# Kernel tuning notes

Hardware: AMD Instinct MI355X
Metric: run time of the kernel (lower is better)

## Reference

```python
import jax, jax.numpy as jnp
import numpy as np

N = 50000
E = 800000
IN_DIM = 128
HID = 128
HEADS = 8
OUT_DIM = 64
NEG_SLOPE = 0.2


def setup_inputs() -> dict:
    key = jax.random.key(0)
    ks = jax.random.split(key, 10)
    x = jax.random.normal(ks[0], (N, IN_DIM), dtype=jnp.float32)
    edge_index = jax.random.randint(ks[1], (2, E), 0, N, dtype=jnp.int64)
    c1 = HID // HEADS  # 16 per-head channels, layer 1
    # layer 1 params (GATConv: lin has no bias; att_src/att_dst are [1,H,C])
    W1 = jax.random.normal(ks[2], (IN_DIM, HEADS * c1), dtype=jnp.float32) * 0.1
    att_src1 = jax.random.normal(ks[3], (1, HEADS, c1), dtype=jnp.float32) * 0.1
    att_dst1 = jax.random.normal(ks[4], (1, HEADS, c1), dtype=jnp.float32) * 0.1
    b1 = jnp.zeros((HEADS * c1,), dtype=jnp.float32)  # concat=True -> bias size H*C
    # layer 2 params (heads=1, concat=False)
    W2 = jax.random.normal(ks[5], (HID, OUT_DIM), dtype=jnp.float32) * 0.1
    att_src2 = jax.random.normal(ks[6], (1, 1, OUT_DIM), dtype=jnp.float32) * 0.1
    att_dst2 = jax.random.normal(ks[7], (1, 1, OUT_DIM), dtype=jnp.float32) * 0.1
    b2 = jnp.zeros((OUT_DIM,), dtype=jnp.float32)
    return {"x": x, "edge_index": edge_index,
            "W1": W1, "att_src1": att_src1, "att_dst1": att_dst1, "b1": b1,
            "W2": W2, "att_src2": att_src2, "att_dst2": att_dst2, "b2": b2}


def _gat_conv(x, src, dst, W, att_src, att_dst, bias, heads, concat):
    n = x.shape[0]
    c = W.shape[1] // heads
    h = (x @ W).reshape(n, heads, c)                      # [N,H,C]
    a_src = jnp.sum(h * att_src, axis=-1)                 # [N,H]
    a_dst = jnp.sum(h * att_dst, axis=-1)                 # [N,H]
    e = a_src[src] + a_dst[dst]                           # [E,H]
    e = jnp.where(e > 0, e, NEG_SLOPE * e)                # leaky_relu
    # segment softmax over incoming edges of each dst node
    m = jax.ops.segment_max(e, dst, num_segments=n)       # [N,H]
    ex = jnp.exp(e - m[dst])
    denom = jax.ops.segment_sum(ex, dst, num_segments=n)  # [N,H]
    alpha = ex / (denom[dst] + 1e-16)                     # [E,H]
    msg = h[src] * alpha[:, :, None]                      # [E,H,C]
    out = jax.ops.segment_sum(msg, dst, num_segments=n)   # [N,H,C]
    out = out.reshape(n, heads * c) if concat else out.mean(axis=1)
    return out + bias


def reference(x, edge_index, W1, att_src1, att_dst1, b1, W2, att_src2, att_dst2, b2):
    # add self-loops (PyG GATConv default add_self_loops=True)
    loops = jnp.arange(N, dtype=edge_index.dtype)
    src = jnp.concatenate([edge_index[0], loops])
    dst = jnp.concatenate([edge_index[1], loops])
    h = _gat_conv(x, src, dst, W1, att_src1, att_dst1, b1, HEADS, True)
    h = jax.nn.elu(h)
    out = _gat_conv(h, src, dst, W2, att_src2, att_dst2, b2, 1, False)
    return jax.nn.log_softmax(out, axis=1)
```

## Files before the change

### kernel.cpp

```cpp
#include <hip/hip_runtime.h>
#include <math.h>

#define N_NODES 50000
#define E_EDGES 800000
#define ET      (E_EDGES + N_NODES)
#define IN_DIM  128
#define HID     128
#define HEADS   8
#define C1      16
#define OUT_DIM 64
#define NEG_SLOPE 0.2f
#define LOG2E   1.4426950408889634f

#define TILE    8192
#define NT      ((ET + TILE - 1) / TILE)
#define NB      ((N_NODES + 255) / 256)

#define CONV_BLOCKS (N_NODES * IN_DIM / 4 / 256)
#define PREP_BLOCKS 112
#define MEGA_A (NT + CONV_BLOCKS + PREP_BLOCKS)
#define L1T_BLOCKS ((N_NODES + 63) / 64)
#define MEGA_B (NB + L1T_BLOCKS)

typedef unsigned int uint32;
typedef __attribute__((ext_vector_type(8))) short bf16x8;
typedef __attribute__((ext_vector_type(4))) float f32x4;

static __device__ __forceinline__ unsigned short f2bf(float f) {
    uint32 u = __float_as_uint(f);
    u += 0x7FFFu + ((u >> 16) & 1u);
    return (unsigned short)(u >> 16);
}


__global__ __launch_bounds__(256) void prep_all(
        const int* __restrict__ dst, int* __restrict__ cnt,
        const float* __restrict__ x, unsigned short* __restrict__ xb,
        const float* __restrict__ W1, const float* __restrict__ as1,
        const float* __restrict__ ad1, const float* __restrict__ W2,
        const float* __restrict__ as2, const float* __restrict__ ad2,
        unsigned short* __restrict__ w1t, unsigned short* __restrict__ p1t,
        unsigned short* __restrict__ w2t, unsigned short* __restrict__ p2t) {
    __shared__ int hist[NB];
    int blk = blockIdx.x, t = threadIdx.x;
    if (blk < NT) {
        for (int b = t; b < NB; b += 256) hist[b] = 0;
        __syncthreads();
        int base = blk * TILE;
        #pragma unroll
        for (int it = 0; it < TILE / 256; ++it) {
            int i = base + it * 256 + t;
            if (i < ET) {
                int d = (i < E_EDGES) ? dst[i] : (i - E_EDGES);
                atomicAdd(&hist[d >> 8], 1);
            }
        }
        __syncthreads();
        for (int b = t; b < NB; b += 256) cnt[blk * NB + b] = hist[b];
    } else if (blk < NT + CONV_BLOCKS) {
        int i = (blk - NT) * 256 + t;
        float4 v = ((const float4*)x)[i];
        ushort4 o;
        o.x = f2bf(v.x); o.y = f2bf(v.y); o.z = f2bf(v.z); o.w = f2bf(v.w);
        ((ushort4*)xb)[i] = o;
    } else {
        int b = blk - NT - CONV_BLOCKS;
        if (b < 64) {
            int i = b * 256 + t;
            int n = i >> 7, k = i & 127;
            w1t[n * IN_DIM + k] = f2bf(W1[k * HID + n]);
        } else if (b < 96) {
            int i = (b - 64) * 256 + t;
            int n = i >> 7, k = i & 127;
            w2t[n * HID + k] = f2bf(W2[k * OUT_DIM + n]);
        } else if (b < 104) {
            int i = (b - 96) * 256 + t;
            int j = i >> 7, k = i & 127;
            int hh = j & 7;
            const float* a = (j < 8) ? as1 : ad1;
            float acc = 0.f;
            #pragma unroll
            for (int c = 0; c < C1; ++c)
                acc = fmaf(W1[k * HID + hh * C1 + c], a[hh * C1 + c], acc);
            p1t[j * IN_DIM + k] = f2bf(acc * LOG2E);
        } else {
            int i = (b - 104) * 256 + t;
            int j = i >> 7, k = i & 127;
            if (j < 2) {
                const float* a = (j == 0) ? as2 : ad2;
                float acc = 0.f;
                #pragma unroll
                for (int c = 0; c < OUT_DIM; ++c)
                    acc = fmaf(W2[k * OUT_DIM + c], a[c], acc);
                p2t[j * HID + k] = f2bf(acc * LOG2E);
            } else {
                p2t[j * HID + k] = 0;
            }
        }
    }
}

__global__ __launch_bounds__(256) void bucket_scan(
        const int* __restrict__ cnt, int* __restrict__ tileOff ,
        int* __restrict__ bucketStart ) {
    __shared__ int s[256];
    int t = threadIdx.x;
    int total = 0;
    if (t < NB) {
        int run = 0;
        for (int k = 0; k < NT; ++k) {
            int c = cnt[k * NB + t];
            tileOff[k * NB + t] = run;
            run += c;
        }
        total = run;
    }
    s[t] = total;
    __syncthreads();
    #pragma unroll
    for (int off = 1; off < 256; off <<= 1) {
        int add = (t >= off) ? s[t - off] : 0;
        __syncthreads();
        s[t] += add;
        __syncthreads();
    }
    if (t < NB) bucketStart[t] = s[t] - total;
    if (t == 0) bucketStart[NB] = ET;
}

__global__ __launch_bounds__(256) void bucket_scatter(
        const int* __restrict__ src, const int* __restrict__ dst,
        const int* __restrict__ tileOff, const int* __restrict__ bucketStart,
        int2* __restrict__ pairs) {
    __shared__ int cur[NB];
    int t = threadIdx.x;
    for (int b = t; b < NB; b += 256)
        cur[b] = bucketStart[b] + tileOff[blockIdx.x * NB + b];
    __syncthreads();
    int base = blockIdx.x * TILE;
    #pragma unroll
    for (int it = 0; it < TILE / 256; ++it) {
        int i = base + it * 256 + t;
        if (i < ET) {
            int s, d;
            if (i < E_EDGES) { s = src[i]; d = dst[i]; }
            else             { s = d = i - E_EDGES; }
            int pos = atomicAdd(&cur[d >> 8], 1);
            pairs[pos] = make_int2(s, d);
        }
    }
}


__global__ __launch_bounds__(256) void build_l1t(
        const int2* __restrict__ pairs, const int* __restrict__ bucketStart,
        int* __restrict__ row_start, int* __restrict__ csr_src,
        const unsigned short* __restrict__ xb, const unsigned short* __restrict__ w1t,
        const unsigned short* __restrict__ p1t, unsigned short* __restrict__ h1b,
        float* __restrict__ a_src, float* __restrict__ a_dst) {
    __shared__ int sdeg[256];
    __shared__ int sscan[256];
    int t = threadIdx.x;
    if (blockIdx.x < NB) {
        int b = blockIdx.x;
        int beg = bucketStart[b], end = bucketStart[b + 1];
        sdeg[t] = 0;
        __syncthreads();
        for (int j = beg + t; j < end; j += 256)
            atomicAdd(&sdeg[pairs[j].y & 255], 1);
        __syncthreads();
        int v = sdeg[t];
        sscan[t] = v;
        __syncthreads();
        #pragma unroll
        for (int off = 1; off < 256; off <<= 1) {
            int add = (t >= off) ? sscan[t - off] : 0;
            __syncthreads();
            sscan[t] += add;
            __syncthreads();
        }
        int pos0 = beg + sscan[t] - v;
        int n = b * 256 + t;
        if (n < N_NODES) row_start[n] = pos0;
        if (b == 0 && t == 0) row_start[N_NODES] = ET;
        __syncthreads();
        sscan[t] = pos0;
        __syncthreads();
        for (int j = beg + t; j < end; j += 256) {
            int2 p = pairs[j];
            int pos = atomicAdd(&sscan[p.y & 255], 1);
            csr_src[pos] = p.x;
        }
        return;
    }
    int bb = blockIdx.x - NB;
    int w = t >> 6, lane = t & 63;
    int l15 = lane & 15, quad = lane >> 4;
    int n0 = bb * 64 + w * 16;
    int mrow = n0 + l15;
    int mload = (mrow < N_NODES) ? mrow : (N_NODES - 1);

    bf16x8 af[4];
    #pragma unroll
    for (int s = 0; s < 4; ++s)
        af[s] = *(const bf16x8*)&xb[(size_t)mload * IN_DIM + s * 32 + quad * 8];

    #pragma unroll
    for (int tt = 0; tt < 9; ++tt) {
        const unsigned short* Brow = (tt < 8) ? &w1t[(tt * 16 + l15) * IN_DIM]
                                              : &p1t[l15 * IN_DIM];
        f32x4 acc = {0.f, 0.f, 0.f, 0.f};
        #pragma unroll
        for (int s = 0; s < 4; ++s) {
            bf16x8 bf = *(const bf16x8*)&Brow[s * 32 + quad * 8];
            acc = __builtin_amdgcn_mfma_f32_16x16x32_bf16(af[s], bf, acc, 0, 0, 0);
        }
        int nodeb = n0 + quad * 4;
        if (tt < 8) {
            int ch = tt * 16 + l15;
            #pragma unroll
            for (int r = 0; r < 4; ++r)
                if (nodeb + r < N_NODES)
                    h1b[(size_t)(nodeb + r) * HID + ch] = f2bf(acc[r]);
        } else {
            #pragma unroll
            for (int r = 0; r < 4; ++r) {
                if (nodeb + r < N_NODES) {
                    if (l15 < 8) a_src[(nodeb + r) * HEADS + l15] = acc[r];
                    else         a_dst[(nodeb + r) * HEADS + (l15 - 8)] = acc[r];
                }
            }
        }
    }
}


__global__ __launch_bounds__(128) void l1_aggregate(
        const unsigned short* __restrict__ h1b, const float* __restrict__ a_src,
        const float* __restrict__ a_dst, const int* __restrict__ row_start,
        const int* __restrict__ csr_src, const float* __restrict__ b1,
        unsigned short* __restrict__ h_act_b) {
    int w = threadIdx.x >> 6;
    int lane = threadIdx.x & 63;
    int n = blockIdx.x * 2 + w;
    int c0 = lane * 2;
    int h = lane >> 3;
    int beg = row_start[n], end = row_start[n + 1];
    float adst = a_dst[n * HEADS + h];
    float l = 0.f, accx = 0.f, accy = 0.f;

    auto update = [&](float e, uint32 u) {
        float vx = __uint_as_float(u << 16);
        float vy = __uint_as_float(u & 0xFFFF0000u);
        e += adst;
        e = fmaxf(e, NEG_SLOPE * e);
        float p = exp2f(e);
        l += p;
        accx = fmaf(p, vx, accx);
        accy = fmaf(p, vy, accy);
    };

    int j = beg;
    for (; j + 8 <= end; j += 8) {
        int ss[8];
        #pragma unroll
        for (int q = 0; q < 8; ++q) ss[q] = csr_src[j + q];
        float ee[8]; uint32 uu[8];
        #pragma unroll
        for (int q = 0; q < 8; ++q) ee[q] = a_src[ss[q] * HEADS + h];
        #pragma unroll
        for (int q = 0; q < 8; ++q) uu[q] = *(const uint32*)&h1b[(size_t)ss[q] * HID + c0];
        #pragma unroll
        for (int q = 0; q < 8; ++q) update(ee[q], uu[q]);
    }
    for (; j + 4 <= end; j += 4) {
        int ss[4];
        #pragma unroll
        for (int q = 0; q < 4; ++q) ss[q] = csr_src[j + q];
        float ee[4]; uint32 uu[4];
        #pragma unroll
        for (int q = 0; q < 4; ++q) ee[q] = a_src[ss[q] * HEADS + h];
        #pragma unroll
        for (int q = 0; q < 4; ++q) uu[q] = *(const uint32*)&h1b[(size_t)ss[q] * HID + c0];
        #pragma unroll
        for (int q = 0; q < 4; ++q) update(ee[q], uu[q]);
    }
    for (; j < end; ++j) {
        int s = csr_src[j];
        float e = a_src[s * HEADS + h];
        uint32 u = *(const uint32*)&h1b[(size_t)s * HID + c0];
        update(e, u);
    }

    float inv = 1.f / (l + 1e-16f);
    float vx = accx * inv + b1[c0];
    float vy = accy * inv + b1[c0 + 1];
    vx = vx > 0.f ? vx : (__expf(vx) - 1.f);
    vy = vy > 0.f ? vy : (__expf(vy) - 1.f);
    uint32 packed = (uint32)f2bf(vx) | ((uint32)f2bf(vy) << 16);
    *(uint32*)&h_act_b[(size_t)n * HID + c0] = packed;
}


__global__ __launch_bounds__(256) void l2_transform_mfma(
        const unsigned short* __restrict__ h_act_b, const unsigned short* __restrict__ w2t,
        const unsigned short* __restrict__ p2t, unsigned short* __restrict__ h2b,
        float* __restrict__ a_src2, float* __restrict__ a_dst2) {
    int t = threadIdx.x, w = t >> 6, lane = t & 63;
    int l15 = lane & 15, quad = lane >> 4;
    int n0 = blockIdx.x * 64 + w * 16;
    int mrow = n0 + l15;
    int mload = (mrow < N_NODES) ? mrow : (N_NODES - 1);

    bf16x8 af[4];
    #pragma unroll
    for (int s = 0; s < 4; ++s)
        af[s] = *(const bf16x8*)&h_act_b[(size_t)mload * HID + s * 32 + quad * 8];

    #pragma unroll
    for (int tt = 0; tt < 5; ++tt) {
        const unsigned short* Brow = (tt < 4) ? &w2t[(tt * 16 + l15) * HID]
                                              : &p2t[l15 * HID];
        f32x4 acc = {0.f, 0.f, 0.f, 0.f};
        #pragma unroll
        for (int s = 0; s < 4; ++s) {
            bf16x8 bf = *(const bf16x8*)&Brow[s * 32 + quad * 8];
            acc = __builtin_amdgcn_mfma_f32_16x16x32_bf16(af[s], bf, acc, 0, 0, 0);
        }
        int nodeb = n0 + quad * 4;
        if (tt < 4) {
            int ch = tt * 16 + l15;
            #pragma unroll
            for (int r = 0; r < 4; ++r)
                if (nodeb + r < N_NODES)
                    h2b[(size_t)(nodeb + r) * OUT_DIM + ch] = f2bf(acc[r]);
        } else {
            #pragma unroll
            for (int r = 0; r < 4; ++r) {
                if (nodeb + r < N_NODES) {
                    if (l15 == 0) a_src2[nodeb + r] = acc[r];
                    else if (l15 == 1) a_dst2[nodeb + r] = acc[r];
                }
            }
        }
    }
}


__global__ __launch_bounds__(128) void l2_aggregate(
        const unsigned short* __restrict__ h2b, const float* __restrict__ a_src2,
        const float* __restrict__ a_dst2, const int* __restrict__ row_start,
        const int* __restrict__ csr_src, const float* __restrict__ b2,
        float* __restrict__ out) {
    int w = threadIdx.x >> 6;
    int lane = threadIdx.x & 63;
    int n = blockIdx.x * 2 + w;
    int beg = row_start[n], end = row_start[n + 1];
    float adst = a_dst2[n];
    float l = 0.f, acc = 0.f;

    auto update = [&](float e, unsigned short us) {
        float v = __uint_as_float(((uint32)us) << 16);
        e += adst;
        e = fmaxf(e, NEG_SLOPE * e);
        float p = exp2f(e);
        l += p;
        acc = fmaf(p, v, acc);
    };

    int j = beg;
    for (; j + 8 <= end; j += 8) {
        int ss[8];
        #pragma unroll
        for (int q = 0; q < 8; ++q) ss[q] = csr_src[j + q];
        float ee[8]; unsigned short vv[8];
        #pragma unroll
        for (int q = 0; q < 8; ++q) ee[q] = a_src2[ss[q]];
        #pragma unroll
        for (int q = 0; q < 8; ++q) vv[q] = h2b[(size_t)ss[q] * OUT_DIM + lane];
        #pragma unroll
        for (int q = 0; q < 8; ++q) update(ee[q], vv[q]);
    }
    for (; j + 4 <= end; j += 4) {
        int ss[4];
        #pragma unroll
        for (int q = 0; q < 4; ++q) ss[q] = csr_src[j + q];
        float ee[4]; unsigned short vv[4];
        #pragma unroll
        for (int q = 0; q < 4; ++q) ee[q] = a_src2[ss[q]];
        #pragma unroll
        for (int q = 0; q < 4; ++q) vv[q] = h2b[(size_t)ss[q] * OUT_DIM + lane];
        #pragma unroll
        for (int q = 0; q < 4; ++q) update(ee[q], vv[q]);
    }
    for (; j < end; ++j) {
        int s = csr_src[j];
        update(a_src2[s], h2b[(size_t)s * OUT_DIM + lane]);
    }

    float o = acc / (l + 1e-16f) + b2[lane];
    float mx = o;
    #pragma unroll
    for (int ww = 32; ww > 0; ww >>= 1) mx = fmaxf(mx, __shfl_xor(mx, ww, 64));
    float ex = __expf(o - mx);
    float ssum = ex;
    #pragma unroll
    for (int ww = 32; ww > 0; ww >>= 1) ssum += __shfl_xor(ssum, ww, 64);
    out[(size_t)n * OUT_DIM + lane] = o - mx - __logf(ssum);
}


extern "C" void kernel_launch(void* const* d_in, const int* in_sizes, int n_in,
                              void* d_out, int out_size, void* d_ws, size_t ws_size,
                              hipStream_t stream) {
    const float* x   = (const float*)d_in[0];
    const int*   ei  = (const int*)d_in[1];
    const float* W1  = (const float*)d_in[2];
    const float* as1 = (const float*)d_in[3];
    const float* ad1 = (const float*)d_in[4];
    const float* b1  = (const float*)d_in[5];
    const float* W2  = (const float*)d_in[6];
    const float* as2 = (const float*)d_in[7];
    const float* ad2 = (const float*)d_in[8];
    const float* b2  = (const float*)d_in[9];
    float* out = (float*)d_out;

    const int* src = ei;
    const int* dst = ei + E_EDGES;

    char* ws = (char*)d_ws;
    size_t off = 0;
    auto alloc = [&](size_t bytes) -> void* {
        void* p = ws + off;
        off += (bytes + 255) & ~size_t(255);
        return p;
    };
    unsigned short* xb     = (unsigned short*)alloc((size_t)N_NODES * IN_DIM * 2);
    unsigned short* h1b    = (unsigned short*)alloc((size_t)N_NODES * HID * 2);
    unsigned short* h_act_b= (unsigned short*)alloc((size_t)N_NODES * HID * 2);
    unsigned short* h2b    = (unsigned short*)alloc((size_t)N_NODES * OUT_DIM * 2);
    unsigned short* w1t    = (unsigned short*)alloc((size_t)HID * IN_DIM * 2);
    unsigned short* p1t    = (unsigned short*)alloc((size_t)16 * IN_DIM * 2);
    unsigned short* w2t    = (unsigned short*)alloc((size_t)OUT_DIM * HID * 2);
    unsigned short* p2t    = (unsigned short*)alloc((size_t)16 * HID * 2);
    float* a_src1    = (float*)alloc((size_t)N_NODES * HEADS * 4);
    float* a_dst1    = (float*)alloc((size_t)N_NODES * HEADS * 4);
    float* a_src2    = (float*)alloc((size_t)N_NODES * 4);
    float* a_dst2    = (float*)alloc((size_t)N_NODES * 4);
    int*   row_start = (int*)alloc((size_t)(N_NODES + 1) * 4);
    int*   csr_src   = (int*)alloc((size_t)ET * 4);
    int2*  pairs     = (int2*)alloc((size_t)ET * 8);
    int*   cnt       = (int*)alloc((size_t)NB * NT * 4);
    int*   tileOff   = (int*)alloc((size_t)NB * NT * 4);
    int*   bucketStart = (int*)alloc((size_t)(NB + 1) * 4);

    prep_all<<<MEGA_A, 256, 0, stream>>>(dst, cnt, x, xb, W1, as1, ad1,
                                         W2, as2, ad2, w1t, p1t, w2t, p2t);
    bucket_scan<<<1, 256, 0, stream>>>(cnt, tileOff, bucketStart);
    bucket_scatter<<<NT, 256, 0, stream>>>(src, dst, tileOff, bucketStart, pairs);
    build_l1t<<<MEGA_B, 256, 0, stream>>>(pairs, bucketStart, row_start, csr_src,
                                          xb, w1t, p1t, h1b, a_src1, a_dst1);
    l1_aggregate<<<N_NODES / 2, 128, 0, stream>>>(h1b, a_src1, a_dst1, row_start, csr_src, b1, h_act_b);
    l2_transform_mfma<<<L1T_BLOCKS, 256, 0, stream>>>(h_act_b, w2t, p2t, h2b, a_src2, a_dst2);
    l2_aggregate<<<N_NODES / 2, 128, 0, stream>>>(h2b, a_src2, a_dst2, row_start, csr_src, b2, out);
}
```

Baseline: 232.7 us.

## Stage bucket scatter in LDS, pack edge pairs, scalarize CSR indices

```diff
diff --git a/kernel.cpp b/kernel.cpp
--- a/kernel.cpp
+++ b/kernel.cpp
@@ -128,16 +128,48 @@
     if (t == 0) bucketStart[NB] = ET;
 }
 
+
 __global__ __launch_bounds__(256) void bucket_scatter(
         const int* __restrict__ src, const int* __restrict__ dst,
         const int* __restrict__ tileOff, const int* __restrict__ bucketStart,
-        int2* __restrict__ pairs) {
-    __shared__ int cur[NB];
+        uint32* __restrict__ pairs) {
+    __shared__ uint32 buf[TILE];
+    __shared__ unsigned char bkt[TILE];
+    __shared__ int lhist[256];
+    __shared__ int lcur[NB];
+    __shared__ int goff[NB];
     int t = threadIdx.x;
-    for (int b = t; b < NB; b += 256)
-        cur[b] = bucketStart[b] + tileOff[blockIdx.x * NB + b];
-    __syncthreads();
     int base = blockIdx.x * TILE;
+
+    lhist[t] = 0;
+    __syncthreads();
+    #pragma unroll
+    for (int it = 0; it < TILE / 256; ++it) {
+        int i = base + it * 256 + t;
+        if (i < ET) {
+            int d = (i < E_EDGES) ? dst[i] : (i - E_EDGES);
+            atomicAdd(&lhist[d >> 8], 1);
+        }
+    }
+    __syncthreads();
+    int v = lhist[t];
+    __syncthreads();
+    lhist[t] = v;
+    __syncthreads();
+    #pragma unroll
+    for (int off = 1; off < 256; off <<= 1) {
+        int add = (t >= off) ? lhist[t - off] : 0;
+        __syncthreads();
+        lhist[t] += add;
+        __syncthreads();
+    }
+    int lstart = lhist[t] - v;
+    int totalCnt = lhist[255];
+    if (t < NB) {
+        lcur[t] = lstart;
+        goff[t] = bucketStart[t] + tileOff[blockIdx.x * NB + t] - lstart;
+    }
+    __syncthreads();
     #pragma unroll
     for (int it = 0; it < TILE / 256; ++it) {
         int i = base + it * 256 + t;
@@ -145,15 +177,20 @@
             int s, d;
             if (i < E_EDGES) { s = src[i]; d = dst[i]; }
             else             { s = d = i - E_EDGES; }
-            int pos = atomicAdd(&cur[d >> 8], 1);
-            pairs[pos] = make_int2(s, d);
-        }
-    }
+            int b = d >> 8;
+            int pos = atomicAdd(&lcur[b], 1);
+            buf[pos] = ((uint32)s << 8) | (uint32)(d & 255);
+            bkt[pos] = (unsigned char)b;
+        }
+    }
+    __syncthreads();
+    for (int i = t; i < totalCnt; i += 256)
+        pairs[goff[bkt[i]] + i] = buf[i];
 }
 
 
 __global__ __launch_bounds__(256) void build_l1t(
-        const int2* __restrict__ pairs, const int* __restrict__ bucketStart,
+        const uint32* __restrict__ pairs, const int* __restrict__ bucketStart,
         int* __restrict__ row_start, int* __restrict__ csr_src,
         const unsigned short* __restrict__ xb, const unsigned short* __restrict__ w1t,
         const unsigned short* __restrict__ p1t, unsigned short* __restrict__ h1b,
@@ -167,7 +204,7 @@
         sdeg[t] = 0;
         __syncthreads();
         for (int j = beg + t; j < end; j += 256)
-            atomicAdd(&sdeg[pairs[j].y & 255], 1);
+            atomicAdd(&sdeg[pairs[j] & 255u], 1);
         __syncthreads();
         int v = sdeg[t];
         sscan[t] = v;
@@ -187,9 +224,9 @@
         sscan[t] = pos0;
         __syncthreads();
         for (int j = beg + t; j < end; j += 256) {
-            int2 p = pairs[j];
-            int pos = atomicAdd(&sscan[p.y & 255], 1);
-            csr_src[pos] = p.x;
+            uint32 p = pairs[j];
+            int pos = atomicAdd(&sscan[p & 255u], 1);
+            csr_src[pos] = (int)(p >> 8);
         }
         return;
     }
@@ -264,7 +301,8 @@
     for (; j + 8 <= end; j += 8) {
         int ss[8];
         #pragma unroll
-        for (int q = 0; q < 8; ++q) ss[q] = csr_src[j + q];
+        for (int q = 0; q < 8; ++q)
+            ss[q] = __builtin_amdgcn_readfirstlane(csr_src[j + q]);
         float ee[8]; uint32 uu[8];
         #pragma unroll
         for (int q = 0; q < 8; ++q) ee[q] = a_src[ss[q] * HEADS + h];
@@ -273,20 +311,8 @@
         #pragma unroll
         for (int q = 0; q < 8; ++q) update(ee[q], uu[q]);
     }
-    for (; j + 4 <= end; j += 4) {
-        int ss[4];
-        #pragma unroll
-        for (int q = 0; q < 4; ++q) ss[q] = csr_src[j + q];
-        float ee[4]; uint32 uu[4];
-        #pragma unroll
-        for (int q = 0; q < 4; ++q) ee[q] = a_src[ss[q] * HEADS + h];
-        #pragma unroll
-        for (int q = 0; q < 4; ++q) uu[q] = *(const uint32*)&h1b[(size_t)ss[q] * HID + c0];
-        #pragma unroll
-        for (int q = 0; q < 4; ++q) update(ee[q], uu[q]);
-    }
     for (; j < end; ++j) {
-        int s = csr_src[j];
+        int s = __builtin_amdgcn_readfirstlane(csr_src[j]);
         float e = a_src[s * HEADS + h];
         uint32 u = *(const uint32*)&h1b[(size_t)s * HID + c0];
         update(e, u);
@@ -372,7 +398,8 @@
     for (; j + 8 <= end; j += 8) {
         int ss[8];
         #pragma unroll
-        for (int q = 0; q < 8; ++q) ss[q] = csr_src[j + q];
+        for (int q = 0; q < 8; ++q)
+            ss[q] = __builtin_amdgcn_readfirstlane(csr_src[j + q]);
         float ee[8]; unsigned short vv[8];
         #pragma unroll
         for (int q = 0; q < 8; ++q) ee[q] = a_src2[ss[q]];
@@ -381,20 +408,8 @@
         #pragma unroll
         for (int q = 0; q < 8; ++q) update(ee[q], vv[q]);
     }
-    for (; j + 4 <= end; j += 4) {
-        int ss[4];
-        #pragma unroll
-        for (int q = 0; q < 4; ++q) ss[q] = csr_src[j + q];
-        float ee[4]; unsigned short vv[4];
-        #pragma unroll
-        for (int q = 0; q < 4; ++q) ee[q] = a_src2[ss[q]];
-        #pragma unroll
-        for (int q = 0; q < 4; ++q) vv[q] = h2b[(size_t)ss[q] * OUT_DIM + lane];
-        #pragma unroll
-        for (int q = 0; q < 4; ++q) update(ee[q], vv[q]);
-    }
     for (; j < end; ++j) {
-        int s = csr_src[j];
+        int s = __builtin_amdgcn_readfirstlane(csr_src[j]);
         update(a_src2[s], h2b[(size_t)s * OUT_DIM + lane]);
     }
 
@@ -449,7 +464,7 @@
     float* a_dst2    = (float*)alloc((size_t)N_NODES * 4);
     int*   row_start = (int*)alloc((size_t)(N_NODES + 1) * 4);
     int*   csr_src   = (int*)alloc((size_t)ET * 4);
-    int2*  pairs     = (int2*)alloc((size_t)ET * 8);
+    uint32* pairs    = (uint32*)alloc((size_t)ET * 4);
     int*   cnt       = (int*)alloc((size_t)NB * NT * 4);
     int*   tileOff   = (int*)alloc((size_t)NB * NT * 4);
     int*   bucketStart = (int*)alloc((size_t)(NB + 1) * 4);
```

Result: slower. 249.4 us (+7.2%).

## Merge all seven stage kernels into one persistent cooperative kernel

Applied to the files above, without the earlier changes.

```diff
diff --git a/kernel.cpp b/kernel.cpp
--- a/kernel.cpp
+++ b/kernel.cpp
@@ -1,5 +1,8 @@
 #include <hip/hip_runtime.h>
+#include <hip/hip_cooperative_groups.h>
 #include <math.h>
+
+namespace cg = cooperative_groups;
 
 #define N_NODES 50000
 #define E_EDGES 800000
@@ -32,381 +35,371 @@
     return (unsigned short)(u >> 16);
 }
 
-
-__global__ __launch_bounds__(256) void prep_all(
-        const int* __restrict__ dst, int* __restrict__ cnt,
-        const float* __restrict__ x, unsigned short* __restrict__ xb,
-        const float* __restrict__ W1, const float* __restrict__ as1,
-        const float* __restrict__ ad1, const float* __restrict__ W2,
-        const float* __restrict__ as2, const float* __restrict__ ad2,
-        unsigned short* __restrict__ w1t, unsigned short* __restrict__ p1t,
-        unsigned short* __restrict__ w2t, unsigned short* __restrict__ p2t) {
-    __shared__ int hist[NB];
-    int blk = blockIdx.x, t = threadIdx.x;
-    if (blk < NT) {
-        for (int b = t; b < NB; b += 256) hist[b] = 0;
+struct MegaParams {
+    const int* src; const int* dst;
+    const float* x;
+    const float* W1; const float* as1; const float* ad1; const float* b1;
+    const float* W2; const float* as2; const float* ad2; const float* b2;
+    float* out;
+    unsigned short* xb; unsigned short* h1b; unsigned short* h_act_b; unsigned short* h2b;
+    unsigned short* w1t; unsigned short* p1t; unsigned short* w2t; unsigned short* p2t;
+    float* a_src1; float* a_dst1; float* a_src2; float* a_dst2;
+    int* row_start; int* csr_src; int2* pairs;
+    int* cnt; int* tileOff; int* bucketStart;
+};
+
+__global__ __launch_bounds__(256) void mega(MegaParams P) {
+    cg::grid_group grid = cg::this_grid();
+    const int t = threadIdx.x;
+    const int G = gridDim.x;
+    __shared__ int sm1[256];
+    __shared__ int sm2[256];
+
+    for (int blk = blockIdx.x; blk < MEGA_A; blk += G) {
+        if (blk < NT) {
+            __syncthreads();
+            for (int b = t; b < NB; b += 256) sm1[b] = 0;
+            __syncthreads();
+            int base = blk * TILE;
+            #pragma unroll
+            for (int it = 0; it < TILE / 256; ++it) {
+                int i = base + it * 256 + t;
+                if (i < ET) {
+                    int d = (i < E_EDGES) ? P.dst[i] : (i - E_EDGES);
+                    atomicAdd(&sm1[d >> 8], 1);
+                }
+            }
+            __syncthreads();
+            for (int b = t; b < NB; b += 256) P.cnt[blk * NB + b] = sm1[b];
+        } else if (blk < NT + CONV_BLOCKS) {
+            int i = (blk - NT) * 256 + t;
+            float4 v = ((const float4*)P.x)[i];
+            ushort4 o;
+            o.x = f2bf(v.x); o.y = f2bf(v.y); o.z = f2bf(v.z); o.w = f2bf(v.w);
+            ((ushort4*)P.xb)[i] = o;
+        } else {
+            int b = blk - NT - CONV_BLOCKS;
+            if (b < 64) {
+                int i = b * 256 + t;
+                int n = i >> 7, k = i & 127;
+                P.w1t[n * IN_DIM + k] = f2bf(P.W1[k * HID + n]);
+            } else if (b < 96) {
+                int i = (b - 64) * 256 + t;
+                int n = i >> 7, k = i & 127;
+                P.w2t[n * HID + k] = f2bf(P.W2[k * OUT_DIM + n]);
+            } else if (b < 104) {
+                int i = (b - 96) * 256 + t;
+                int j = i >> 7, k = i & 127;
+                int hh = j & 7;
+                const float* a = (j < 8) ? P.as1 : P.ad1;
+                float acc = 0.f;
+                #pragma unroll
+                for (int c = 0; c < C1; ++c)
+                    acc = fmaf(P.W1[k * HID + hh * C1 + c], a[hh * C1 + c], acc);
+                P.p1t[j * IN_DIM + k] = f2bf(acc * LOG2E);
+            } else {
+                int i = (b - 104) * 256 + t;
+                int j = i >> 7, k = i & 127;
+                if (j < 2) {
+                    const float* a = (j == 0) ? P.as2 : P.ad2;
+                    float acc = 0.f;
+                    #pragma unroll
+                    for (int c = 0; c < OUT_DIM; ++c)
+                        acc = fmaf(P.W2[k * OUT_DIM + c], a[c], acc);
+                    P.p2t[j * HID + k] = f2bf(acc * LOG2E);
+                } else {
+                    P.p2t[j * HID + k] = 0;
+                }
+            }
+        }
+    }
+    grid.sync();
+
+    if (blockIdx.x == 0) {
+        int total = 0;
+        if (t < NB) {
+            int run = 0;
+            for (int k = 0; k < NT; ++k) {
+                int c = P.cnt[k * NB + t];
+                P.tileOff[k * NB + t] = run;
+                run += c;
+            }
+            total = run;
+        }
+        sm1[t] = total;
         __syncthreads();
-        int base = blk * TILE;
+        #pragma unroll
+        for (int off = 1; off < 256; off <<= 1) {
+            int add = (t >= off) ? sm1[t - off] : 0;
+            __syncthreads();
+            sm1[t] += add;
+            __syncthreads();
+        }
+        if (t < NB) P.bucketStart[t] = sm1[t] - total;
+        if (t == 0) P.bucketStart[NB] = ET;
+    }
+    grid.sync();
+
+    for (int tile = blockIdx.x; tile < NT; tile += G) {
+        __syncthreads();
+        for (int b = t; b < NB; b += 256)
+            sm1[b] = P.bucketStart[b] + P.tileOff[tile * NB + b];
+        __syncthreads();
+        int base = tile * TILE;
         #pragma unroll
         for (int it = 0; it < TILE / 256; ++it) {
             int i = base + it * 256 + t;
             if (i < ET) {
-                int d = (i < E_EDGES) ? dst[i] : (i - E_EDGES);
-                atomicAdd(&hist[d >> 8], 1);
-            }
-        }
-        __syncthreads();
-        for (int b = t; b < NB; b += 256) cnt[blk * NB + b] = hist[b];
-    } else if (blk < NT + CONV_BLOCKS) {
-        int i = (blk - NT) * 256 + t;
-        float4 v = ((const float4*)x)[i];
-        ushort4 o;
-        o.x = f2bf(v.x); o.y = f2bf(v.y); o.z = f2bf(v.z); o.w = f2bf(v.w);
-        ((ushort4*)xb)[i] = o;
-    } else {
-        int b = blk - NT - CONV_BLOCKS;
-        if (b < 64) {
-            int i = b * 256 + t;
-            int n = i >> 7, k = i & 127;
-            w1t[n * IN_DIM + k] = f2bf(W1[k * HID + n]);
-        } else if (b < 96) {
-            int i = (b - 64) * 256 + t;
-            int n = i >> 7, k = i & 127;
-            w2t[n * HID + k] = f2bf(W2[k * OUT_DIM + n]);
-        } else if (b < 104) {
-            int i = (b - 96) * 256 + t;
-            int j = i >> 7, k = i & 127;
-            int hh = j & 7;
-            const float* a = (j < 8) ? as1 : ad1;
-            float acc = 0.f;
-            #pragma unroll
-            for (int c = 0; c < C1; ++c)
-                acc = fmaf(W1[k * HID + hh * C1 + c], a[hh * C1 + c], acc);
-            p1t[j * IN_DIM + k] = f2bf(acc * LOG2E);
+                int s, d;
+                if (i < E_EDGES) { s = P.src[i]; d = P.dst[i]; }
+                else             { s = d = i - E_EDGES; }
+                int pos = atomicAdd(&sm1[d >> 8], 1);
+                P.pairs[pos] = make_int2(s, d);
+            }
+        }
+    }
+    grid.sync();
+
+    for (int u = blockIdx.x; u < MEGA_B; u += G) {
+        if (u < NB) {
+            __syncthreads();
+            int b = u;
+            int beg = P.bucketStart[b], end = P.bucketStart[b + 1];
+            sm1[t] = 0;
+            __syncthreads();
+            for (int j = beg + t; j < end; j += 256)
+                atomicAdd(&sm1[P.pairs[j].y & 255], 1);
+            __syncthreads();
+            int v = sm1[t];
+            sm2[t] = v;
+            __syncthreads();
+            #pragma unroll
+            for (int off = 1; off < 256; off <<= 1) {
+                int add = (t >= off) ? sm2[t - off] : 0;
+                __syncthreads();
+                sm2[t] += add;
+                __syncthreads();
+            }
+            int pos0 = beg + sm2[t] - v;
+            int n = b * 256 + t;
+            if (n < N_NODES) P.row_start[n] = pos0;
+            if (b == 0 && t == 0) P.row_start[N_NODES] = ET;
+            __syncthreads();
+            sm2[t] = pos0;
+            __syncthreads();
+            for (int j = beg + t; j < end; j += 256) {
+                int2 p = P.pairs[j];
+                int pos = atomicAdd(&sm2[p.y & 255], 1);
+                P.csr_src[pos] = p.x;
+            }
         } else {
-            int i = (b - 104) * 256 + t;
-            int j = i >> 7, k = i & 127;
-            if (j < 2) {
-                const float* a = (j == 0) ? as2 : ad2;
-                float acc = 0.f;
-                #pragma unroll
-                for (int c = 0; c < OUT_DIM; ++c)
-                    acc = fmaf(W2[k * OUT_DIM + c], a[c], acc);
-                p2t[j * HID + k] = f2bf(acc * LOG2E);
+            int bb = u - NB;
+            int w = t >> 6, lane = t & 63;
+            int l15 = lane & 15, quad = lane >> 4;
+            int n0 = bb * 64 + w * 16;
+            int mrow = n0 + l15;
+            int mload = (mrow < N_NODES) ? mrow : (N_NODES - 1);
+
+            bf16x8 af[4];
+            #pragma unroll
+            for (int s = 0; s < 4; ++s)
+                af[s] = *(const bf16x8*)&P.xb[(size_t)mload * IN_DIM + s * 32 + quad * 8];
+
+            #pragma unroll
+            for (int tt = 0; tt < 9; ++tt) {
+                const unsigned short* Brow = (tt < 8) ? &P.w1t[(tt * 16 + l15) * IN_DIM]
+                                                      : &P.p1t[l15 * IN_DIM];
+                f32x4 acc = {0.f, 0.f, 0.f, 0.f};
+                #pragma unroll
+                for (int s = 0; s < 4; ++s) {
+                    bf16x8 bf = *(const bf16x8*)&Brow[s * 32 + quad * 8];
+                    acc = __builtin_amdgcn_mfma_f32_16x16x32_bf16(af[s], bf, acc, 0, 0, 0);
+                }
+                int nodeb = n0 + quad * 4;
+                if (tt < 8) {
+                    int ch = tt * 16 + l15;
+                    #pragma unroll
+                    for (int r = 0; r < 4; ++r)
+                        if (nodeb + r < N_NODES)
+                            P.h1b[(size_t)(nodeb + r) * HID + ch] = f2bf(acc[r]);
+                } else {
+                    #pragma unroll
+                    for (int r = 0; r < 4; ++r) {
+                        if (nodeb + r < N_NODES) {
+                            if (l15 < 8) P.a_src1[(nodeb + r) * HEADS + l15] = acc[r];
+                            else         P.a_dst1[(nodeb + r) * HEADS + (l15 - 8)] = acc[r];
+                        }
+                    }
+                }
+            }
+        }
+    }
+    grid.sync();
+
+    {
+        int w = t >> 6, lane = t & 63;
+        int c0 = lane * 2;
+        int h = lane >> 3;
+        for (int g5 = blockIdx.x; g5 < N_NODES / 4; g5 += G) {
+            int n = g5 * 4 + w;
+            int beg = P.row_start[n], end = P.row_start[n + 1];
+            float adst = P.a_dst1[n * HEADS + h];
+            float l = 0.f, accx = 0.f, accy = 0.f;
+
+            auto update = [&](float e, uint32 u) {
+                float vx = __uint_as_float(u << 16);
+                float vy = __uint_as_float(u & 0xFFFF0000u);
+                e += adst;
+                e = fmaxf(e, NEG_SLOPE * e);
+                float p = exp2f(e);
+                l += p;
+                accx = fmaf(p, vx, accx);
+                accy = fmaf(p, vy, accy);
+            };
+
+            int j = beg;
+            for (; j + 8 <= end; j += 8) {
+                int ss[8];
+                #pragma unroll
+                for (int q = 0; q < 8; ++q) ss[q] = P.csr_src[j + q];
+                float ee[8]; uint32 uu[8];
+                #pragma unroll
+                for (int q = 0; q < 8; ++q) ee[q] = P.a_src1[ss[q] * HEADS + h];
+                #pragma unroll
+                for (int q = 0; q < 8; ++q) uu[q] = *(const uint32*)&P.h1b[(size_t)ss[q] * HID + c0];
+                #pragma unroll
+                for (int q = 0; q < 8; ++q) update(ee[q], uu[q]);
+            }
+            for (; j + 4 <= end; j += 4) {
+                int ss[4];
+                #pragma unroll
+                for (int q = 0; q < 4; ++q) ss[q] = P.csr_src[j + q];
+                float ee[4]; uint32 uu[4];
+                #pragma unroll
+                for (int q = 0; q < 4; ++q) ee[q] = P.a_src1[ss[q] * HEADS + h];
+                #pragma unroll
+                for (int q = 0; q < 4; ++q) uu[q] = *(const uint32*)&P.h1b[(size_t)ss[q] * HID + c0];
+                #pragma unroll
+                for (int q = 0; q < 4; ++q) update(ee[q], uu[q]);
+            }
+            for (; j < end; ++j) {
+                int s = P.csr_src[j];
+                float e = P.a_src1[s * HEADS + h];
+                uint32 u = *(const uint32*)&P.h1b[(size_t)s * HID + c0];
+                update(e, u);
+            }
+
+            float inv = 1.f / (l + 1e-16f);
+            float vx = accx * inv + P.b1[c0];
+            float vy = accy * inv + P.b1[c0 + 1];
+            vx = vx > 0.f ? vx : (__expf(vx) - 1.f);
+            vy = vy > 0.f ? vy : (__expf(vy) - 1.f);
+            uint32 packed = (uint32)f2bf(vx) | ((uint32)f2bf(vy) << 16);
+            *(uint32*)&P.h_act_b[(size_t)n * HID + c0] = packed;
+        }
+    }
+    grid.sync();
+
+    for (int u = blockIdx.x; u < L1T_BLOCKS; u += G) {
+        int w = t >> 6, lane = t & 63;
+        int l15 = lane & 15, quad = lane >> 4;
+        int n0 = u * 64 + w * 16;
+        int mrow = n0 + l15;
+        int mload = (mrow < N_NODES) ? mrow : (N_NODES - 1);
+
+        bf16x8 af[4];
+        #pragma unroll
+        for (int s = 0; s < 4; ++s)
+            af[s] = *(const bf16x8*)&P.h_act_b[(size_t)mload * HID + s * 32 + quad * 8];
+
+        #pragma unroll
+        for (int tt = 0; tt < 5; ++tt) {
+            const unsigned short* Brow = (tt < 4) ? &P.w2t[(tt * 16 + l15) * HID]
+                                                  : &P.p2t[l15 * HID];
+            f32x4 acc = {0.f, 0.f, 0.f, 0.f};
+            #pragma unroll
+            for (int s = 0; s < 4; ++s) {
+                bf16x8 bf = *(const bf16x8*)&Brow[s * 32 + quad * 8];
+                acc = __builtin_amdgcn_mfma_f32_16x16x32_bf16(af[s], bf, acc, 0, 0, 0);
+            }
+            int nodeb = n0 + quad * 4;
+            if (tt < 4) {
+                int ch = tt * 16 + l15;
+                #pragma unroll
+                for (int r = 0; r < 4; ++r)
+                    if (nodeb + r < N_NODES)
+                        P.h2b[(size_t)(nodeb + r) * OUT_DIM + ch] = f2bf(acc[r]);
             } else {
-                p2t[j * HID + k] = 0;
-            }
-        }
-    }
-}
-
-__global__ __launch_bounds__(256) void bucket_scan(
-        const int* __restrict__ cnt, int* __restrict__ tileOff ,
-        int* __restrict__ bucketStart ) {
-    __shared__ int s[256];
-    int t = threadIdx.x;
-    int total = 0;
-    if (t < NB) {
-        int run = 0;
-        for (int k = 0; k < NT; ++k) {
-            int c = cnt[k * NB + t];
-            tileOff[k * NB + t] = run;
-            run += c;
-        }
-        total = run;
-    }
-    s[t] = total;
-    __syncthreads();
-    #pragma unroll
-    for (int off = 1; off < 256; off <<= 1) {
-        int add = (t >= off) ? s[t - off] : 0;
-        __syncthreads();
-        s[t] += add;
-        __syncthreads();
-    }
-    if (t < NB) bucketStart[t] = s[t] - total;
-    if (t == 0) bucketStart[NB] = ET;
-}
-
-__global__ __launch_bounds__(256) void bucket_scatter(
-        const int* __restrict__ src, const int* __restrict__ dst,
-        const int* __restrict__ tileOff, const int* __restrict__ bucketStart,
-        int2* __restrict__ pairs) {
-    __shared__ int cur[NB];
-    int t = threadIdx.x;
-    for (int b = t; b < NB; b += 256)
-        cur[b] = bucketStart[b] + tileOff[blockIdx.x * NB + b];
-    __syncthreads();
-    int base = blockIdx.x * TILE;
-    #pragma unroll
-    for (int it = 0; it < TILE / 256; ++it) {
-        int i = base + it * 256 + t;
-        if (i < ET) {
-            int s, d;
-            if (i < E_EDGES) { s = src[i]; d = dst[i]; }
-            else             { s = d = i - E_EDGES; }
-            int pos = atomicAdd(&cur[d >> 8], 1);
-            pairs[pos] = make_int2(s, d);
-        }
-    }
-}
-
-
-__global__ __launch_bounds__(256) void build_l1t(
-        const int2* __restrict__ pairs, const int* __restrict__ bucketStart,
-        int* __restrict__ row_start, int* __restrict__ csr_src,
-        const unsigned short* __restrict__ xb, const unsigned short* __restrict__ w1t,
-        const unsigned short* __restrict__ p1t, unsigned short* __restrict__ h1b,
-        float* __restrict__ a_src, float* __restrict__ a_dst) {
-    __shared__ int sdeg[256];
-    __shared__ int sscan[256];
-    int t = threadIdx.x;
-    if (blockIdx.x < NB) {
-        int b = blockIdx.x;
-        int beg = bucketStart[b], end = bucketStart[b + 1];
-        sdeg[t] = 0;
-        __syncthreads();
-        for (int j = beg + t; j < end; j += 256)
-            atomicAdd(&sdeg[pairs[j].y & 255], 1);
-        __syncthreads();
-        int v = sdeg[t];
-        sscan[t] = v;
-        __syncthreads();
-        #pragma unroll
-        for (int off = 1; off < 256; off <<= 1) {
-            int add = (t >= off) ? sscan[t - off] : 0;
-            __syncthreads();
-            sscan[t] += add;
-            __syncthreads();
-        }
-        int pos0 = beg + sscan[t] - v;
-        int n = b * 256 + t;
-        if (n < N_NODES) row_start[n] = pos0;
-        if (b == 0 && t == 0) row_start[N_NODES] = ET;
-        __syncthreads();
-        sscan[t] = pos0;
-        __syncthreads();
-        for (int j = beg + t; j < end; j += 256) {
-            int2 p = pairs[j];
-            int pos = atomicAdd(&sscan[p.y & 255], 1);
-            csr_src[pos] = p.x;
-        }
-        return;
-    }
-    int bb = blockIdx.x - NB;
-    int w = t >> 6, lane = t & 63;
-    int l15 = lane & 15, quad = lane >> 4;
-    int n0 = bb * 64 + w * 16;
-    int mrow = n0 + l15;
-    int mload = (mrow < N_NODES) ? mrow : (N_NODES - 1);
-
-    bf16x8 af[4];
-    #pragma unroll
-    for (int s = 0; s < 4; ++s)
-        af[s] = *(const bf16x8*)&xb[(size_t)mload * IN_DIM + s * 32 + quad * 8];
-
-    #pragma unroll
-    for (int tt = 0; tt < 9; ++tt) {
-        const unsigned short* Brow = (tt < 8) ? &w1t[(tt * 16 + l15) * IN_DIM]
-                                              : &p1t[l15 * IN_DIM];
-        f32x4 acc = {0.f, 0.f, 0.f, 0.f};
-        #pragma unroll
-        for (int s = 0; s < 4; ++s) {
-            bf16x8 bf = *(const bf16x8*)&Brow[s * 32 + quad * 8];
-            acc = __builtin_amdgcn_mfma_f32_16x16x32_bf16(af[s], bf, acc, 0, 0, 0);
-        }
-        int nodeb = n0 + quad * 4;
-        if (tt < 8) {
-            int ch = tt * 16 + l15;
-            #pragma unroll
-            for (int r = 0; r < 4; ++r)
-                if (nodeb + r < N_NODES)
-                    h1b[(size_t)(nodeb + r) * HID + ch] = f2bf(acc[r]);
-        } else {
-            #pragma unroll
-            for (int r = 0; r < 4; ++r) {
-                if (nodeb + r < N_NODES) {
-                    if (l15 < 8) a_src[(nodeb + r) * HEADS + l15] = acc[r];
-                    else         a_dst[(nodeb + r) * HEADS + (l15 - 8)] = acc[r];
+                #pragma unroll
+                for (int r = 0; r < 4; ++r) {
+                    if (nodeb + r < N_NODES) {
+                        if (l15 == 0) P.a_src2[nodeb + r] = acc[r];
+                        else if (l15 == 1) P.a_dst2[nodeb + r] = acc[r];
+                    }
                 }
             }
         }
     }
-}
-
-
-__global__ __launch_bounds__(128) void l1_aggregate(
-        const unsigned short* __restrict__ h1b, const float* __restrict__ a_src,
-        const float* __restrict__ a_dst, const int* __restrict__ row_start,
-        const int* __restrict__ csr_src, const float* __restrict__ b1,
-        unsigned short* __restrict__ h_act_b) {
-    int w = threadIdx.x >> 6;
-    int lane = threadIdx.x & 63;
-    int n = blockIdx.x * 2 + w;
-    int c0 = lane * 2;
-    int h = lane >> 3;
-    int beg = row_start[n], end = row_start[n + 1];
-    float adst = a_dst[n * HEADS + h];
-    float l = 0.f, accx = 0.f, accy = 0.f;
-
-    auto update = [&](float e, uint32 u) {
-        float vx = __uint_as_float(u << 16);
-        float vy = __uint_as_float(u & 0xFFFF0000u);
-        e += adst;
-        e = fmaxf(e, NEG_SLOPE * e);
-        float p = exp2f(e);
-        l += p;
-        accx = fmaf(p, vx, accx);
-        accy = fmaf(p, vy, accy);
-    };
-
-    int j = beg;
-    for (; j + 8 <= end; j += 8) {
-        int ss[8];
-        #pragma unroll
-        for (int q = 0; q < 8; ++q) ss[q] = csr_src[j + q];
-        float ee[8]; uint32 uu[8];
-        #pragma unroll
-        for (int q = 0; q < 8; ++q) ee[q] = a_src[ss[q] * HEADS + h];
-        #pragma unroll
-        for (int q = 0; q < 8; ++q) uu[q] = *(const uint32*)&h1b[(size_t)ss[q] * HID + c0];
-        #pragma unroll
-        for (int q = 0; q < 8; ++q) update(ee[q], uu[q]);
-    }
-    for (; j + 4 <= end; j += 4) {
-        int ss[4];
-        #pragma unroll
-        for (int q = 0; q < 4; ++q) ss[q] = csr_src[j + q];
-        float ee[4]; uint32 uu[4];
-        #pragma unroll
-        for (int q = 0; q < 4; ++q) ee[q] = a_src[ss[q] * HEADS + h];
-        #pragma unroll
-        for (int q = 0; q < 4; ++q) uu[q] = *(const uint32*)&h1b[(size_t)ss[q] * HID + c0];
-        #pragma unroll
-        for (int q = 0; q < 4; ++q) update(ee[q], uu[q]);
-    }
-    for (; j < end; ++j) {
-        int s = csr_src[j];
-        float e = a_src[s * HEADS + h];
-        uint32 u = *(const uint32*)&h1b[(size_t)s * HID + c0];
-        update(e, u);
-    }
-
-    float inv = 1.f / (l + 1e-16f);
-    float vx = accx * inv + b1[c0];
-    float vy = accy * inv + b1[c0 + 1];
-    vx = vx > 0.f ? vx : (__expf(vx) - 1.f);
-    vy = vy > 0.f ? vy : (__expf(vy) - 1.f);
-    uint32 packed = (uint32)f2bf(vx) | ((uint32)f2bf(vy) << 16);
-    *(uint32*)&h_act_b[(size_t)n * HID + c0] = packed;
-}
-
-
-__global__ __launch_bounds__(256) void l2_transform_mfma(
-        const unsigned short* __restrict__ h_act_b, const unsigned short* __restrict__ w2t,
-        const unsigned short* __restrict__ p2t, unsigned short* __restrict__ h2b,
-        float* __restrict__ a_src2, float* __restrict__ a_dst2) {
-    int t = threadIdx.x, w = t >> 6, lane = t & 63;
-    int l15 = lane & 15, quad = lane >> 4;
-    int n0 = blockIdx.x * 64 + w * 16;
-    int mrow = n0 + l15;
-    int mload = (mrow < N_NODES) ? mrow : (N_NODES - 1);
-
-    bf16x8 af[4];
-    #pragma unroll
-    for (int s = 0; s < 4; ++s)
-        af[s] = *(const bf16x8*)&h_act_b[(size_t)mload * HID + s * 32 + quad * 8];
-
-    #pragma unroll
-    for (int tt = 0; tt < 5; ++tt) {
-        const unsigned short* Brow = (tt < 4) ? &w2t[(tt * 16 + l15) * HID]
-                                              : &p2t[l15 * HID];
-        f32x4 acc = {0.f, 0.f, 0.f, 0.f};
-        #pragma unroll
-        for (int s = 0; s < 4; ++s) {
-            bf16x8 bf = *(const bf16x8*)&Brow[s * 32 + quad * 8];
-            acc = __builtin_amdgcn_mfma_f32_16x16x32_bf16(af[s], bf, acc, 0, 0, 0);
-        }
-        int nodeb = n0 + quad * 4;
-        if (tt < 4) {
-            int ch = tt * 16 + l15;
-            #pragma unroll
-            for (int r = 0; r < 4; ++r)
-                if (nodeb + r < N_NODES)
-                    h2b[(size_t)(nodeb + r) * OUT_DIM + ch] = f2bf(acc[r]);
-        } else {
-            #pragma unroll
-            for (int r = 0; r < 4; ++r) {
-                if (nodeb + r < N_NODES) {
-                    if (l15 == 0) a_src2[nodeb + r] = acc[r];
-                    else if (l15 == 1) a_dst2[nodeb + r] = acc[r];
-                }
-            }
-        }
-    }
-}
-
-
-__global__ __launch_bounds__(128) void l2_aggregate(
-        const unsigned short* __restrict__ h2b, const float* __restrict__ a_src2,
-        const float* __restrict__ a_dst2, const int* __restrict__ row_start,
-        const int* __restrict__ csr_src, const float* __restrict__ b2,
-        float* __restrict__ out) {
-    int w = threadIdx.x >> 6;
-    int lane = threadIdx.x & 63;
-    int n = blockIdx.x * 2 + w;
-    int beg = row_start[n], end = row_start[n + 1];
-    float adst = a_dst2[n];
-    float l = 0.f, acc = 0.f;
-
-    auto update = [&](float e, unsigned short us) {
-        float v = __uint_as_float(((uint32)us) << 16);
-        e += adst;
-        e = fmaxf(e, NEG_SLOPE * e);
-        float p = exp2f(e);
-        l += p;
-        acc = fmaf(p, v, acc);
-    };
-
-    int j = beg;
-    for (; j + 8 <= end; j += 8) {
-        int ss[8];
-        #pragma unroll
-        for (int q = 0; q < 8; ++q) ss[q] = csr_src[j + q];
-        float ee[8]; unsigned short vv[8];
-        #pragma unroll
-        for (int q = 0; q < 8; ++q) ee[q] = a_src2[ss[q]];
-        #pragma unroll
-        for (int q = 0; q < 8; ++q) vv[q] = h2b[(size_t)ss[q] * OUT_DIM + lane];
-        #pragma unroll
-        for (int q = 0; q < 8; ++q) update(ee[q], vv[q]);
-    }
-    for (; j + 4 <= end; j += 4) {
-        int ss[4];
-        #pragma unroll
-        for (int q = 0; q < 4; ++q) ss[q] = csr_src[j + q];
-        float ee[4]; unsigned short vv[4];
-        #pragma unroll
-        for (int q = 0; q < 4; ++q) ee[q] = a_src2[ss[q]];
-        #pragma unroll
-        for (int q = 0; q < 4; ++q) vv[q] = h2b[(size_t)ss[q] * OUT_DIM + lane];
-        #pragma unroll
-        for (int q = 0; q < 4; ++q) update(ee[q], vv[q]);
-    }
-    for (; j < end; ++j) {
-        int s = csr_src[j];
-        update(a_src2[s], h2b[(size_t)s * OUT_DIM + lane]);
-    }
-
-    float o = acc / (l + 1e-16f) + b2[lane];
-    float mx = o;
-    #pragma unroll
-    for (int ww = 32; ww > 0; ww >>= 1) mx = fmaxf(mx, __shfl_xor(mx, ww, 64));
-    float ex = __expf(o - mx);
-    float ssum = ex;
-    #pragma unroll
-    for (int ww = 32; ww > 0; ww >>= 1) ssum += __shfl_xor(ssum, ww, 64);
-    out[(size_t)n * OUT_DIM + lane] = o - mx - __logf(ssum);
+    grid.sync();
+
+    {
+        int w = t >> 6, lane = t & 63;
+        for (int g7 = blockIdx.x; g7 < N_NODES / 4; g7 += G) {
+            int n = g7 * 4 + w;
+            int beg = P.row_start[n], end = P.row_start[n + 1];
+            float adst = P.a_dst2[n];
+            float l = 0.f, acc = 0.f;
+
+            auto update = [&](float e, unsigned short us) {
+                float v = __uint_as_float(((uint32)us) << 16);
+                e += adst;
+                e = fmaxf(e, NEG_SLOPE * e);
+                float p = exp2f(e);
+                l += p;
+                acc = fmaf(p, v, acc);
+            };
+
+            int j = beg;
+            for (; j + 8 <= end; j += 8) {
+                int ss[8];
+                #pragma unroll
+                for (int q = 0; q < 8; ++q) ss[q] = P.csr_src[j + q];
+                float ee[8]; unsigned short vv[8];
+                #pragma unroll
+                for (int q = 0; q < 8; ++q) ee[q] = P.a_src2[ss[q]];
+                #pragma unroll
+                for (int q = 0; q < 8; ++q) vv[q] = P.h2b[(size_t)ss[q] * OUT_DIM + lane];
+                #pragma unroll
+                for (int q = 0; q < 8; ++q) update(ee[q], vv[q]);
+            }
+            for (; j + 4 <= end; j += 4) {
+                int ss[4];
+                #pragma unroll
+                for (int q = 0; q < 4; ++q) ss[q] = P.csr_src[j + q];
+                float ee[4]; unsigned short vv[4];
+                #pragma unroll
+                for (int q = 0; q < 4; ++q) ee[q] = P.a_src2[ss[q]];
+                #pragma unroll
+                for (int q = 0; q < 4; ++q) vv[q] = P.h2b[(size_t)ss[q] * OUT_DIM + lane];
+                #pragma unroll
+                for (int q = 0; q < 4; ++q) update(ee[q], vv[q]);
+            }
+            for (; j < end; ++j) {
+                int s = P.csr_src[j];
+                update(P.a_src2[s], P.h2b[(size_t)s * OUT_DIM + lane]);
+            }
+
+            float o = acc / (l + 1e-16f) + P.b2[lane];
+            float mx = o;
+            #pragma unroll
+            for (int ww = 32; ww > 0; ww >>= 1) mx = fmaxf(mx, __shfl_xor(mx, ww, 64));
+            float ex = __expf(o - mx);
+            float ssum = ex;
+            #pragma unroll
+            for (int ww = 32; ww > 0; ww >>= 1) ssum += __shfl_xor(ssum, ww, 64);
+            P.out[(size_t)n * OUT_DIM + lane] = o - mx - __logf(ssum);
+        }
+    }
 }
 
 
@@ -425,9 +418,6 @@
     const float* b2  = (const float*)d_in[9];
     float* out = (float*)d_out;
 
-    const int* src = ei;
-    const int* dst = ei + E_EDGES;
-
     char* ws = (char*)d_ws;
     size_t off = 0;
     auto alloc = [&](size_t bytes) -> void* {
@@ -435,32 +425,37 @@
         off += (bytes + 255) & ~size_t(255);
         return p;
     };
-    unsigned short* xb     = (unsigned short*)alloc((size_t)N_NODES * IN_DIM * 2);
-    unsigned short* h1b    = (unsigned short*)alloc((size_t)N_NODES * HID * 2);
-    unsigned short* h_act_b= (unsigned short*)alloc((size_t)N_NODES * HID * 2);
-    unsigned short* h2b    = (unsigned short*)alloc((size_t)N_NODES * OUT_DIM * 2);
-    unsigned short* w1t    = (unsigned short*)alloc((size_t)HID * IN_DIM * 2);
-    unsigned short* p1t    = (unsigned short*)alloc((size_t)16 * IN_DIM * 2);
-    unsigned short* w2t    = (unsigned short*)alloc((size_t)OUT_DIM * HID * 2);
-    unsigned short* p2t    = (unsigned short*)alloc((size_t)16 * HID * 2);
-    float* a_src1    = (float*)alloc((size_t)N_NODES * HEADS * 4);
-    float* a_dst1    = (float*)alloc((size_t)N_NODES * HEADS * 4);
-    float* a_src2    = (float*)alloc((size_t)N_NODES * 4);
-    float* a_dst2    = (float*)alloc((size_t)N_NODES * 4);
-    int*   row_start = (int*)alloc((size_t)(N_NODES + 1) * 4);
-    int*   csr_src   = (int*)alloc((size_t)ET * 4);
-    int2*  pairs     = (int2*)alloc((size_t)ET * 8);
-    int*   cnt       = (int*)alloc((size_t)NB * NT * 4);
-    int*   tileOff   = (int*)alloc((size_t)NB * NT * 4);
-    int*   bucketStart = (int*)alloc((size_t)(NB + 1) * 4);
-
-    prep_all<<<MEGA_A, 256, 0, stream>>>(dst, cnt, x, xb, W1, as1, ad1,
-                                         W2, as2, ad2, w1t, p1t, w2t, p2t);
-    bucket_scan<<<1, 256, 0, stream>>>(cnt, tileOff, bucketStart);
-    bucket_scatter<<<NT, 256, 0, stream>>>(src, dst, tileOff, bucketStart, pairs);
-    build_l1t<<<MEGA_B, 256, 0, stream>>>(pairs, bucketStart, row_start, csr_src,
-                                          xb, w1t, p1t, h1b, a_src1, a_dst1);
-    l1_aggregate<<<N_NODES / 2, 128, 0, stream>>>(h1b, a_src1, a_dst1, row_start, csr_src, b1, h_act_b);
-    l2_transform_mfma<<<L1T_BLOCKS, 256, 0, stream>>>(h_act_b, w2t, p2t, h2b, a_src2, a_dst2);
-    l2_aggregate<<<N_NODES / 2, 128, 0, stream>>>(h2b, a_src2, a_dst2, row_start, csr_src, b2, out);
+    MegaParams P;
+    P.src = ei;
+    P.dst = ei + E_EDGES;
+    P.x = x; P.W1 = W1; P.as1 = as1; P.ad1 = ad1; P.b1 = b1;
+    P.W2 = W2; P.as2 = as2; P.ad2 = ad2; P.b2 = b2;
+    P.out = out;
+    P.xb      = (unsigned short*)alloc((size_t)N_NODES * IN_DIM * 2);
+    P.h1b     = (unsigned short*)alloc((size_t)N_NODES * HID * 2);
+    P.h_act_b = (unsigned short*)alloc((size_t)N_NODES * HID * 2);
+    P.h2b     = (unsigned short*)alloc((size_t)N_NODES * OUT_DIM * 2);
+    P.w1t     = (unsigned short*)alloc((size_t)HID * IN_DIM * 2);
+    P.p1t     = (unsigned short*)alloc((size_t)16 * IN_DIM * 2);
+    P.w2t     = (unsigned short*)alloc((size_t)OUT_DIM * HID * 2);
+    P.p2t     = (unsigned short*)alloc((size_t)16 * HID * 2);
+    P.a_src1  = (float*)alloc((size_t)N_NODES * HEADS * 4);
+    P.a_dst1  = (float*)alloc((size_t)N_NODES * HEADS * 4);
+    P.a_src2  = (float*)alloc((size_t)N_NODES * 4);
+    P.a_dst2  = (float*)alloc((size_t)N_NODES * 4);
+    P.row_start = (int*)alloc((size_t)(N_NODES + 1) * 4);
+    P.csr_src   = (int*)alloc((size_t)ET * 4);
+    P.pairs     = (int2*)alloc((size_t)ET * 8);
+    P.cnt       = (int*)alloc((size_t)NB * NT * 4);
+    P.tileOff   = (int*)alloc((size_t)NB * NT * 4);
+    P.bucketStart = (int*)alloc((size_t)(NB + 1) * 4);
+
+    int perCU = 0;
+    hipOccupancyMaxActiveBlocksPerMultiprocessor(&perCU, mega, 256, 0);
+    if (perCU < 1) perCU = 1;
+    int G = perCU * 256;
+    if (G > 2048) G = 2048;
+
+    void* args[] = { (void*)&P };
+    hipLaunchCooperativeKernel((const void*)mega, dim3(G), dim3(256), args, 0, stream);
 }
```

New measurement: 655.5 us. 182% more time.
